# Kernel optimization log

Hardware: AMD Instinct MI355X
Metric: run time of the kernel (lower is better)

Reference implementation:

```python
import jax, jax.numpy as jnp
import numpy as np

N_NODES = 50000
N_EDGES = 640000
DIM_V = 128
DIM_E = 128
BN_EPS = 1e-5


def _lrelu(x):
    return jax.nn.leaky_relu(x, 0.2)


def _mlp3(x, W1, b1, W2, b2, W3, b3):
    h = _lrelu(x @ W1 + b1)
    h = _lrelu(h @ W2 + b2)
    return h @ W3 + b3


def _bn_train(x, gamma, beta):
    # BatchNorm1d in training mode: batch stats, biased variance
    m = jnp.mean(x, axis=0)
    v = jnp.mean((x - m) ** 2, axis=0)
    return (x - m) * jax.lax.rsqrt(v + BN_EPS) * gamma + beta


def setup_inputs() -> dict:
    key = jax.random.key(0)
    ks = jax.random.split(key, 20)
    node_fea = jax.random.normal(ks[0], (N_NODES, DIM_V), dtype=jnp.float32)
    edge_fea = jax.random.normal(ks[1], (N_EDGES, DIM_E), dtype=jnp.float32)
    idx1 = jax.random.randint(ks[2], (N_EDGES,), 0, N_NODES)
    idx2 = jax.random.randint(ks[3], (N_EDGES,), 0, N_NODES)
    dt_e = 2 * DIM_V + DIM_E  # phi_e input dim
    dt_v = DIM_V + DIM_E      # phi_v input dim
    s = 0.05
    return {
        "node_fea": node_fea, "edge_fea": edge_fea,
        "idx1": idx1, "idx2": idx2,
        "We1": jax.random.normal(ks[4], (dt_e, DIM_E), jnp.float32) * s,
        "be1": jnp.zeros((DIM_E,), jnp.float32),
        "We2": jax.random.normal(ks[5], (DIM_E, DIM_E), jnp.float32) * s,
        "be2": jnp.zeros((DIM_E,), jnp.float32),
        "We3": jax.random.normal(ks[6], (DIM_E, DIM_E), jnp.float32) * s,
        "be3": jnp.zeros((DIM_E,), jnp.float32),
        "Wv1": jax.random.normal(ks[7], (dt_v, DIM_V), jnp.float32) * s,
        "bv1": jnp.zeros((DIM_V,), jnp.float32),
        "Wv2": jax.random.normal(ks[8], (DIM_V, DIM_V), jnp.float32) * s,
        "bv2": jnp.zeros((DIM_V,), jnp.float32),
        "Wv3": jax.random.normal(ks[9], (DIM_V, DIM_V), jnp.float32) * s,
        "bv3": jnp.zeros((DIM_V,), jnp.float32),
        "gamma_e": jnp.ones((DIM_E,), jnp.float32),
        "beta_e": jnp.zeros((DIM_E,), jnp.float32),
        "gamma_v": jnp.ones((DIM_V,), jnp.float32),
        "beta_v": jnp.zeros((DIM_V,), jnp.float32),
    }


def reference(node_fea, edge_fea, idx1, idx2,
              We1, be1, We2, be2, We3, be3,
              Wv1, bv1, Wv2, bv2, Wv3, bv3,
              gamma_e, beta_e, gamma_v, beta_v):
    n_nodes = node_fea.shape[0]
    # gather endpoints, concat with edge features -> [E, 2*dim_v + dim_e]
    z = jnp.concatenate([node_fea[idx1], node_fea[idx2], edge_fea], axis=1)
    ek_prime = _bn_train(_mlp3(z, We1, be1, We2, be2, We3, be3), gamma_e, beta_e)
    edge_new = edge_fea + ek_prime
    # scatter_mean over idx1 into [N, dim_v]; empty segments stay zero
    seg_sum = jax.ops.segment_sum(ek_prime, idx1, num_segments=n_nodes)
    cnt = jax.ops.segment_sum(jnp.ones((idx1.shape[0], 1), ek_prime.dtype), idx1,
                              num_segments=n_nodes)
    vi_e_bar = seg_sum / jnp.maximum(cnt, 1.0)
    z2 = jnp.concatenate([vi_e_bar, node_fea], axis=1)
    vi_prime = _bn_train(_mlp3(z2, Wv1, bv1, Wv2, bv2, Wv3, bv3), gamma_v, beta_v)
    node_new = node_fea + vi_prime
    return node_new, edge_new
```

## Files before the change

kernel.cpp:

```cpp
#include <hip/hip_runtime.h>
#include <cstddef>

#define BN_EPS 1e-5f
constexpr int NNODES = 50000;
constexpr int NEDGES = 640000;
constexpr int DV = 128;
constexpr int NSLOT_E = 512;
constexpr int NSLOT_V = 256;

typedef __attribute__((ext_vector_type(4))) float f32x4;
typedef __attribute__((ext_vector_type(8))) short s16x8;
typedef unsigned short ushort_t;

__device__ __forceinline__ float lrelu(float x) { return x > 0.f ? x : 0.2f * x; }

__device__ __forceinline__ short f2bf(float f) {
  unsigned int u = __builtin_bit_cast(unsigned int, f);
  u += 0x7fffu + ((u >> 16) & 1u);
  return (short)(u >> 16);
}

__device__ __forceinline__ float bf2f(ushort_t u) {
  return __builtin_bit_cast(float, (unsigned int)u << 16);
}

__global__ __launch_bounds__(256)
void to_bf16(const float* __restrict__ src, ushort_t* __restrict__ dst, int n8) {
  int i = blockIdx.x * 256 + threadIdx.x;
  if (i >= n8) return;
  const float* s = src + (size_t)i * 8;
  float4 x0 = *(const float4*)s;
  float4 x1 = *(const float4*)(s + 4);
  s16x8 v;
  v[0] = f2bf(x0.x); v[1] = f2bf(x0.y); v[2] = f2bf(x0.z); v[3] = f2bf(x0.w);
  v[4] = f2bf(x1.x); v[5] = f2bf(x1.y); v[6] = f2bf(x1.z); v[7] = f2bf(x1.w);
  *(s16x8*)(dst + (size_t)i * 8) = v;
}

__global__ __launch_bounds__(256)
void pack_all(const float* __restrict__ W0, const float* __restrict__ W1,
              const float* __restrict__ W2, const float* __restrict__ W3,
              const float* __restrict__ W4, const float* __restrict__ W5,
              ushort_t* __restrict__ out) {
  int t = blockIdx.x * 256 + threadIdx.x;
  if (t >= 288 * 64) return;
  int lane = t & 63, f = t >> 6;
  const float* W; int lf;
  if (f < 96)       { W = W0; lf = f; }
  else if (f < 128) { W = W1; lf = f - 96; }
  else if (f < 160) { W = W2; lf = f - 128; }
  else if (f < 224) { W = W3; lf = f - 160; }
  else if (f < 256) { W = W4; lf = f - 224; }
  else              { W = W5; lf = f - 256; }
  int kk = lf >> 3, n = lf & 7;
  int k0 = kk * 32 + (lane >> 4) * 8, col = n * 16 + (lane & 15);
  s16x8 v;
#pragma unroll
  for (int j = 0; j < 8; j++) v[j] = f2bf(W[(size_t)(k0 + j) * DV + col]);
  *(s16x8*)(out + (size_t)t * 8) = v;
}

__global__ __launch_bounds__(256)
void csr_hist(const int* __restrict__ idx1, int* __restrict__ deg) {
  int e = blockIdx.x * 256 + threadIdx.x;
  if (e < NEDGES) atomicAdd(&deg[idx1[e]], 1);
}

__global__ __launch_bounds__(256)
void csr_scan(const int* __restrict__ deg, int* __restrict__ row_ptr,
              int* __restrict__ cursor) {
  __shared__ int part[256];
  const int t = threadIdx.x;
  const int CH = (NNODES + 255) / 256;
  int s = 0;
  for (int i = 0; i < CH; i++) { int n = t * CH + i; if (n < NNODES) s += deg[n]; }
  part[t] = s;
  __syncthreads();
  if (t == 0) {
    int run = 0;
    for (int i = 0; i < 256; i++) { int v = part[i]; part[i] = run; run += v; }
  }
  __syncthreads();
  int run = part[t];
  for (int i = 0; i < CH; i++) {
    int n = t * CH + i;
    if (n < NNODES) { row_ptr[n] = run; cursor[n] = run; run += deg[n]; }
  }
}

__global__ __launch_bounds__(256)
void csr_fill(const int* __restrict__ idx1, int* __restrict__ cursor,
              int* __restrict__ eidx) {
  int e = blockIdx.x * 256 + threadIdx.x;
  if (e < NEDGES) {
    int pos = atomicAdd(&cursor[idx1[e]], 1);
    eidx[pos] = e;
  }
}

template<int RS>
__device__ __forceinline__ void mfma_span(const char* Als, const s16x8* __restrict__ Wp,
                                          int fkk0, int nkk, f32x4 acc[2][2],
                                          int lane, int rg, int nh) {
  const int col0 = lane & 15;
  const int kg16 = (lane >> 4) * 16;
  const int sw = (col0 & 7) << 4;
  const int r0 = (rg * 32 + col0) * RS;
  const int r1 = (rg * 32 + 16 + col0) * RS;
#pragma unroll
  for (int kk = 0; kk < nkk; kk++) {
    const int ko = (kk * 64 + kg16) ^ sw;
    s16x8 a0 = *(const s16x8*)(Als + r0 + ko);
    s16x8 a1 = *(const s16x8*)(Als + r1 + ko);
    s16x8 b0 = Wp[(size_t)((fkk0 + kk) * 8 + nh * 2 + 0) * 64 + lane];
    s16x8 b1 = Wp[(size_t)((fkk0 + kk) * 8 + nh * 2 + 1) * 64 + lane];
    acc[0][0] = __builtin_amdgcn_mfma_f32_16x16x32_bf16(a0, b0, acc[0][0], 0, 0, 0);
    acc[0][1] = __builtin_amdgcn_mfma_f32_16x16x32_bf16(a0, b1, acc[0][1], 0, 0, 0);
    acc[1][0] = __builtin_amdgcn_mfma_f32_16x16x32_bf16(a1, b0, acc[1][0], 0, 0, 0);
    acc[1][1] = __builtin_amdgcn_mfma_f32_16x16x32_bf16(a1, b1, acc[1][1], 0, 0, 0);
  }
}

__device__ __forceinline__ void store_h64(char* H, const f32x4 acc[2][2],
                                          const float* __restrict__ bias,
                                          int lane, int rg, int nh) {
  const int col0 = lane & 15, lg = lane >> 4;
#pragma unroll
  for (int ar = 0; ar < 2; ar++) {
#pragma unroll
    for (int n = 0; n < 2; n++) {
      const int col = nh * 32 + n * 16 + col0;
      float bi = bias[col];
#pragma unroll
      for (int r = 0; r < 4; r++) {
        int row = rg * 32 + ar * 16 + lg * 4 + r;
        float v = lrelu(acc[ar][n][r] + bi);
        *(ushort_t*)(H + row * 256 + ((col * 2) ^ ((row & 7) << 4))) = (ushort_t)f2bf(v);
      }
    }
  }
}

__global__ __launch_bounds__(512, 8)
void edge_mlp_mfma(const ushort_t* __restrict__ node_b, const float* __restrict__ edge_fea,
                   const int* __restrict__ idx1, const int* __restrict__ idx2,
                   const ushort_t* __restrict__ Wp1, const float* __restrict__ b1,
                   const ushort_t* __restrict__ Wp2, const float* __restrict__ b2,
                   const ushort_t* __restrict__ Wp3, const float* __restrict__ b3,
                   ushort_t* __restrict__ h3b, float* __restrict__ slots) {
  __shared__ __align__(16) char zsm[64 * 384];
  __shared__ __align__(16) char hb[64 * 256];
  const int tid = threadIdx.x;
  const int lane = tid & 63, wid = tid >> 6;
  const int rg = wid & 1, nh = wid >> 1;
  const int e0 = blockIdx.x * 64;

  for (int t = tid; t < 64 * 24; t += 512) {
    int e = t / 24, p = t % 24;
    int er = e0 + e;
    const ushort_t* src = (p < 16) ? (node_b + (size_t)idx1[er] * DV + p * 8)
                                   : (node_b + (size_t)idx2[er] * DV + (p - 16) * 8);
    s16x8 v = *(const s16x8*)src;
    *(s16x8*)(zsm + e * 384 + ((p * 16) ^ ((e & 7) << 4))) = v;
  }
  __syncthreads();

  f32x4 acc[2][2];
#pragma unroll
  for (int i = 0; i < 2; i++)
#pragma unroll
    for (int j = 0; j < 2; j++) acc[i][j] = 0.0f;

  mfma_span<384>(zsm, (const s16x8*)Wp1, 0, 6, acc, lane, rg, nh);
  __syncthreads();

  for (int t = tid; t < 64 * 24; t += 512) {
    int e = t / 24, p = t % 24;
    int er = e0 + e;
    s16x8 v;
    if (p < 8) {
      v = *(const s16x8*)(node_b + (size_t)idx2[er] * DV + 64 + p * 8);
    } else {
      const float* s = edge_fea + (size_t)er * DV + (p - 8) * 8;
      float4 x0 = *(const float4*)s;
      float4 x1 = *(const float4*)(s + 4);
      v[0] = f2bf(x0.x); v[1] = f2bf(x0.y); v[2] = f2bf(x0.z); v[3] = f2bf(x0.w);
      v[4] = f2bf(x1.x); v[5] = f2bf(x1.y); v[6] = f2bf(x1.z); v[7] = f2bf(x1.w);
    }
    *(s16x8*)(zsm + e * 384 + ((p * 16) ^ ((e & 7) << 4))) = v;
  }
  __syncthreads();

  mfma_span<384>(zsm, (const s16x8*)Wp1, 6, 6, acc, lane, rg, nh);

  store_h64(hb, acc, b1, lane, rg, nh);
  __syncthreads();

#pragma unroll
  for (int i = 0; i < 2; i++)
#pragma unroll
    for (int j = 0; j < 2; j++) acc[i][j] = 0.0f;
  mfma_span<256>(hb, (const s16x8*)Wp2, 0, 4, acc, lane, rg, nh);

  store_h64(zsm, acc, b2, lane, rg, nh);
  __syncthreads();

#pragma unroll
  for (int i = 0; i < 2; i++)
#pragma unroll
    for (int j = 0; j < 2; j++) acc[i][j] = 0.0f;
  mfma_span<256>(zsm, (const s16x8*)Wp3, 0, 4, acc, lane, rg, nh);

  const int col0 = lane & 15, lg = lane >> 4;
  float* ps = (float*)hb;
  float* pq = ps + 16 * DV;
#pragma unroll
  for (int ar = 0; ar < 2; ar++) {
#pragma unroll
    for (int n = 0; n < 2; n++) {
      const int col = nh * 32 + n * 16 + col0;
      float bi = b3[col];
      float s = 0.f, q = 0.f;
#pragma unroll
      for (int r = 0; r < 4; r++) {
        int row = rg * 32 + ar * 16 + lg * 4 + r;
        float v = acc[ar][n][r] + bi;
        h3b[(size_t)(e0 + row) * 256 + col] = (ushort_t)f2bf(v);
        s += v; q += v * v;
      }
      ps[(rg * 8 + ar * 4 + lg) * DV + col] = s;
      pq[(rg * 8 + ar * 4 + lg) * DV + col] = q;
    }
  }
  __syncthreads();
  if (tid < 128) {
    float s = 0.f, q = 0.f;
#pragma unroll
    for (int g = 0; g < 16; g++) { s += ps[g * DV + tid]; q += pq[g * DV + tid]; }
    float* sl = slots + (size_t)(blockIdx.x % NSLOT_E) * 256;
    atomicAdd(sl + tid, s);
    atomicAdd(sl + 128 + tid, q);
  }
}

__global__ __launch_bounds__(256)
void node_gather_fused(const float* __restrict__ edge_fea, const int* __restrict__ row_ptr,
                       const int* __restrict__ deg, const int* __restrict__ eidx,
                       const float* __restrict__ ss, float* eslot,
                       ushort_t* __restrict__ vbar_b) {
  const int n = blockIdx.x * 4 + (threadIdx.x >> 6);
  const int lane = threadIdx.x & 63;
  if (n >= NNODES) return;
  const int start = row_ptr[n], d = deg[n];
  const int j = lane * 2;
  const float sc0 = ss[j], sc1 = ss[j + 1];
  const float sh0 = ss[128 + j], sh1 = ss[129 + j];
  const ushort_t* h3b = (const ushort_t*)eslot;
  float a0 = 0.f, a1 = 0.f;
  int i = 0;
  for (; i + 2 <= d; i += 2) {
    int e0 = eidx[start + i], e1 = eidx[start + i + 1];
    ushort2 u0 = *(const ushort2*)(h3b + (size_t)e0 * 256 + j);
    ushort2 u1 = *(const ushort2*)(h3b + (size_t)e1 * 256 + j);
    float2 f0 = *(const float2*)(edge_fea + (size_t)e0 * DV + j);
    float2 f1 = *(const float2*)(edge_fea + (size_t)e1 * DV + j);
    float h00 = bf2f(u0.x), h01 = bf2f(u0.y);
    float h10 = bf2f(u1.x), h11 = bf2f(u1.y);
    a0 += h00 + h10; a1 += h01 + h11;
    float2 o0, o1;
    o0.x = f0.x + fmaf(h00, sc0, sh0); o0.y = f0.y + fmaf(h01, sc1, sh1);
    o1.x = f1.x + fmaf(h10, sc0, sh0); o1.y = f1.y + fmaf(h11, sc1, sh1);
    *(float2*)(eslot + (size_t)e0 * DV + j) = o0;
    *(float2*)(eslot + (size_t)e1 * DV + j) = o1;
  }
  if (i < d) {
    int e0 = eidx[start + i];
    ushort2 u0 = *(const ushort2*)(h3b + (size_t)e0 * 256 + j);
    float2 f0 = *(const float2*)(edge_fea + (size_t)e0 * DV + j);
    float h00 = bf2f(u0.x), h01 = bf2f(u0.y);
    a0 += h00; a1 += h01;
    float2 o0;
    o0.x = f0.x + fmaf(h00, sc0, sh0); o0.y = f0.y + fmaf(h01, sc1, sh1);
    *(float2*)(eslot + (size_t)e0 * DV + j) = o0;
  }
  float vx, vy;
  if (d > 0) {
    float inv = 1.f / (float)d;
    vx = fmaf(a0 * inv, sc0, sh0);
    vy = fmaf(a1 * inv, sc1, sh1);
  } else {
    vx = 0.f; vy = 0.f;
  }
  ushort2 vb;
  vb.x = (ushort_t)f2bf(vx);
  vb.y = (ushort_t)f2bf(vy);
  *(ushort2*)(vbar_b + (size_t)n * DV + j) = vb;
}

template<int K>
__device__ __forceinline__ void layer_mfma(const char* Als, const s16x8* __restrict__ Wp,
                                           f32x4 acc[4], int lane, int rg, int nh) {
  const int arow = rg * 16 + (lane & 15);
  const int rowoff = arow * (K * 2);
  const int kg16 = (lane >> 4) * 16;
  const int sw = (arow & 7) << 4;
#pragma unroll
  for (int n = 0; n < 4; n++) acc[n] = 0.0f;
#pragma unroll 2
  for (int kk = 0; kk < K / 32; kk++) {
    s16x8 a = *(const s16x8*)(Als + rowoff + ((kk * 64 + kg16) ^ sw));
#pragma unroll
    for (int n = 0; n < 4; n++) {
      s16x8 b = Wp[(size_t)(kk * 8 + nh * 4 + n) * 64 + lane];
      acc[n] = __builtin_amdgcn_mfma_f32_16x16x32_bf16(a, b, acc[n], 0, 0, 0);
    }
  }
}

__device__ __forceinline__ void store_h_lds(char* H, const f32x4 acc[4],
                                            const float* __restrict__ bias,
                                            int lane, int rg, int nh) {
  const int col0 = lane & 15, lg = lane >> 4;
#pragma unroll
  for (int n = 0; n < 4; n++) {
    const int col = nh * 64 + n * 16 + col0;
    float bi = bias[col];
#pragma unroll
    for (int r = 0; r < 4; r++) {
      int row = rg * 16 + lg * 4 + r;
      float v = lrelu(acc[n][r] + bi);
      *(ushort_t*)(H + row * 256 + ((col * 2) ^ ((row & 7) << 4))) = (ushort_t)f2bf(v);
    }
  }
}

__global__ __launch_bounds__(256)
void node_mlp_mfma(const ushort_t* __restrict__ node_b, const ushort_t* __restrict__ vbar_b,
                   const ushort_t* __restrict__ Wp1, const float* __restrict__ b1,
                   const ushort_t* __restrict__ Wp2, const float* __restrict__ b2,
                   const ushort_t* __restrict__ Wp3, const float* __restrict__ b3,
                   float* __restrict__ h_out, float* __restrict__ slots) {
  __shared__ __align__(16) char zsm[32 * 512];
  __shared__ __align__(16) char hb[32 * 256];
  const int tid = threadIdx.x;
  const int lane = tid & 63, wid = tid >> 6;
  const int rg = wid & 1, nh = wid >> 1;
  const int n0 = blockIdx.x * 32;

  for (int t = tid; t < 32 * 32; t += 256) {
    int e = t / 32, p = t % 32;
    int nr = n0 + e;
    s16x8 v = (s16x8)0;
    if (nr < NNODES) {
      const ushort_t* src = (p < 16) ? (vbar_b + (size_t)nr * DV + p * 8)
                                     : (node_b + (size_t)nr * DV + (p - 16) * 8);
      v = *(const s16x8*)src;
    }
    *(s16x8*)(zsm + e * 512 + ((p * 16) ^ ((e & 7) << 4))) = v;
  }
  __syncthreads();

  f32x4 acc[4];

  layer_mfma<256>(zsm, (const s16x8*)Wp1, acc, lane, rg, nh);
  store_h_lds(hb, acc, b1, lane, rg, nh);
  __syncthreads();

  layer_mfma<128>(hb, (const s16x8*)Wp2, acc, lane, rg, nh);
  __syncthreads();
  store_h_lds(zsm, acc, b2, lane, rg, nh);
  __syncthreads();

  layer_mfma<128>(zsm, (const s16x8*)Wp3, acc, lane, rg, nh);

  const int col0 = lane & 15, lg = lane >> 4;
  float* ps = (float*)hb;
  float* pq = (float*)zsm;
#pragma unroll
  for (int n = 0; n < 4; n++) {
    const int col = nh * 64 + n * 16 + col0;
    float bi = b3[col];
    float s = 0.f, q = 0.f;
#pragma unroll
    for (int r = 0; r < 4; r++) {
      int row = rg * 16 + lg * 4 + r;
      int gr = n0 + row;
      if (gr < NNODES) {
        float v = acc[n][r] + bi;
        h_out[(size_t)gr * DV + col] = v;
        s += v; q += v * v;
      }
    }
    ps[(rg * 4 + lg) * DV + col] = s;
    pq[(rg * 4 + lg) * DV + col] = q;
  }
  __syncthreads();
  if (tid < 128) {
    float s = 0.f, q = 0.f;
#pragma unroll
    for (int g = 0; g < 8; g++) { s += ps[g * DV + tid]; q += pq[g * DV + tid]; }
    float* sl = slots + (size_t)(blockIdx.x % NSLOT_V) * 256;
    atomicAdd(sl + tid, s);
    atomicAdd(sl + 128 + tid, q);
  }
}

__global__ __launch_bounds__(256)
void stats_reduce(const float* __restrict__ slots, int nslot, float inv_n,
                  const float* __restrict__ gamma, const float* __restrict__ beta,
                  float* __restrict__ ss) {
  __shared__ float tot[256];
  const int j = threadIdx.x;
  float s = 0.f;
  for (int t = 0; t < nslot; t++) s += slots[(size_t)t * 256 + j];
  tot[j] = s;
  __syncthreads();
  if (j < 128) {
    float mean = tot[j] * inv_n;
    float var = tot[j + 128] * inv_n - mean * mean;
    float rs = rsqrtf(var + BN_EPS);
    float sc = gamma[j] * rs;
    ss[j] = sc;
    ss[128 + j] = beta[j] - mean * sc;
  }
}

__global__ __launch_bounds__(256)
void node_finalize(const float* __restrict__ node_fea, const float* __restrict__ ss,
                   float* __restrict__ h_inout) {
  const size_t base = (size_t)blockIdx.x * 1024 + threadIdx.x * 4;
  const int j = (int)(base & 127);
  float4 h = *(float4*)&h_inout[base];
  float4 nf = *(const float4*)&node_fea[base];
  float4 o;
  o.x = nf.x + fmaf(h.x, ss[j + 0], ss[128 + j + 0]);
  o.y = nf.y + fmaf(h.y, ss[j + 1], ss[128 + j + 1]);
  o.z = nf.z + fmaf(h.z, ss[j + 2], ss[128 + j + 2]);
  o.w = nf.w + fmaf(h.w, ss[j + 3], ss[128 + j + 3]);
  *(float4*)&h_inout[base] = o;
}

extern "C" void kernel_launch(void* const* d_in, const int* in_sizes, int n_in,
                              void* d_out, int out_size, void* d_ws, size_t ws_size,
                              hipStream_t stream) {
  const float* node_fea = (const float*)d_in[0];
  const float* edge_fea = (const float*)d_in[1];
  const int* idx1 = (const int*)d_in[2];
  const int* idx2 = (const int*)d_in[3];
  const float* We1 = (const float*)d_in[4];  const float* be1 = (const float*)d_in[5];
  const float* We2 = (const float*)d_in[6];  const float* be2 = (const float*)d_in[7];
  const float* We3 = (const float*)d_in[8];  const float* be3 = (const float*)d_in[9];
  const float* Wv1 = (const float*)d_in[10]; const float* bv1 = (const float*)d_in[11];
  const float* Wv2 = (const float*)d_in[12]; const float* bv2 = (const float*)d_in[13];
  const float* Wv3 = (const float*)d_in[14]; const float* bv3 = (const float*)d_in[15];
  const float* gamma_e = (const float*)d_in[16]; const float* beta_e = (const float*)d_in[17];
  const float* gamma_v = (const float*)d_in[18]; const float* beta_v = (const float*)d_in[19];

  float* out_node = (float*)d_out;
  float* out_edge = out_node + (size_t)NNODES * DV;

  float* ws = (float*)d_ws;
  size_t o = 0;
  int* deg = (int*)(ws + o);      o += NNODES;
  float* slots_e = ws + o;        o += (size_t)NSLOT_E * 256;
  float* slots_v = ws + o;        o += (size_t)NSLOT_V * 256;
  const size_t zero_bytes = o * sizeof(float);
  int* row_ptr = (int*)(ws + o);  o += NNODES;
  int* cursor = (int*)(ws + o);   o += NNODES;
  int* eidx = (int*)(ws + o);     o += NEDGES;
  float* ss_e = ws + o;           o += 256;
  float* ss_v = ws + o;           o += 256;
  ushort_t* node_b = (ushort_t*)(ws + o);  o += (size_t)NNODES * DV / 2;
  ushort_t* vbar_b = (ushort_t*)(ws + o);  o += (size_t)NNODES * DV / 2;
  ushort_t* wpack = (ushort_t*)(ws + o);

  const ushort_t* Wp_e1 = wpack;
  const ushort_t* Wp_e2 = wpack + (size_t)96 * 512;
  const ushort_t* Wp_e3 = wpack + (size_t)128 * 512;
  const ushort_t* Wp_v1 = wpack + (size_t)160 * 512;
  const ushort_t* Wp_v2 = wpack + (size_t)224 * 512;
  const ushort_t* Wp_v3 = wpack + (size_t)256 * 512;

  hipMemsetAsync(d_ws, 0, zero_bytes, stream);

  to_bf16<<<(NNODES * DV / 8 + 255) / 256, 256, 0, stream>>>(node_fea, node_b, NNODES * DV / 8);
  pack_all<<<72, 256, 0, stream>>>(We1, We2, We3, Wv1, Wv2, Wv3, wpack);
  csr_hist<<<(NEDGES + 255) / 256, 256, 0, stream>>>(idx1, deg);
  csr_scan<<<1, 256, 0, stream>>>(deg, row_ptr, cursor);
  csr_fill<<<(NEDGES + 255) / 256, 256, 0, stream>>>(idx1, cursor, eidx);

  edge_mlp_mfma<<<NEDGES / 64, 512, 0, stream>>>(node_b, edge_fea, idx1, idx2,
                                                 Wp_e1, be1, Wp_e2, be2, Wp_e3, be3,
                                                 (ushort_t*)out_edge, slots_e);
  stats_reduce<<<1, 256, 0, stream>>>(slots_e, NSLOT_E, 1.f / NEDGES, gamma_e, beta_e, ss_e);
  node_gather_fused<<<(NNODES + 3) / 4, 256, 0, stream>>>(edge_fea, row_ptr, deg, eidx,
                                                          ss_e, out_edge, vbar_b);
  node_mlp_mfma<<<(NNODES + 31) / 32, 256, 0, stream>>>(node_b, vbar_b,
                                                        Wp_v1, bv1, Wp_v2, bv2, Wp_v3, bv3,
                                                        out_node, slots_v);
  stats_reduce<<<1, 256, 0, stream>>>(slots_v, NSLOT_V, 1.f / NNODES, gamma_v, beta_v, ss_v);
  node_finalize<<<(NNODES * DV) / 1024, 256, 0, stream>>>(node_fea, ss_v, out_node);
}
```

Measured before the change: 861.2 us.

## Stash bf16 edge features in output slot and use hardware bf16 pack conversion

The edge MLP kernel now writes its bf16-converted edge features into the upper half of each 256-short output row, alongside the bf16 h3. The gather kernel reads them from there instead of re-reading fp32 edge_fea, which cuts its read traffic on the residual path. The software round-to-nearest bf16 conversion is also replaced by the v_cvt_pk_bf16_f32 instruction, with a packed two-value variant. In exchange, the edge residual is now added from a bf16-rounded copy of edge_fea rather than the exact fp32 values, and the edge kernel does an extra global write.

```diff
diff --git a/kernel.cpp b/kernel.cpp
--- a/kernel.cpp
+++ b/kernel.cpp
@@ -14,12 +14,24 @@
 
 __device__ __forceinline__ float lrelu(float x) { return x > 0.f ? x : 0.2f * x; }
 
-__device__ __forceinline__ short f2bf(float f) {
-  unsigned int u = __builtin_bit_cast(unsigned int, f);
-  u += 0x7fffu + ((u >> 16) & 1u);
-  return (short)(u >> 16);
-}
-
+__device__ __forceinline__ unsigned cvt_pk_bf16(float lo, float hi) {
+  unsigned r;
+  asm("v_cvt_pk_bf16_f32 %0, %1, %2" : "=v"(r) : "v"(lo), "v"(hi));
+  return r;
+}
+__device__ __forceinline__ ushort_t f2bf(float f) {
+  unsigned r;
+  asm("v_cvt_pk_bf16_f32 %0, %1, %1" : "=v"(r) : "v"(f));
+  return (ushort_t)r;
+}
+__device__ __forceinline__ s16x8 pack8(float4 a, float4 b) {
+  union { unsigned u[4]; s16x8 v; } r;
+  r.u[0] = cvt_pk_bf16(a.x, a.y);
+  r.u[1] = cvt_pk_bf16(a.z, a.w);
+  r.u[2] = cvt_pk_bf16(b.x, b.y);
+  r.u[3] = cvt_pk_bf16(b.z, b.w);
+  return r.v;
+}
 __device__ __forceinline__ float bf2f(ushort_t u) {
   return __builtin_bit_cast(float, (unsigned int)u << 16);
 }
@@ -31,10 +43,7 @@
   const float* s = src + (size_t)i * 8;
   float4 x0 = *(const float4*)s;
   float4 x1 = *(const float4*)(s + 4);
-  s16x8 v;
-  v[0] = f2bf(x0.x); v[1] = f2bf(x0.y); v[2] = f2bf(x0.z); v[3] = f2bf(x0.w);
-  v[4] = f2bf(x1.x); v[5] = f2bf(x1.y); v[6] = f2bf(x1.z); v[7] = f2bf(x1.w);
-  *(s16x8*)(dst + (size_t)i * 8) = v;
+  *(s16x8*)(dst + (size_t)i * 8) = pack8(x0, x1);
 }
 
 __global__ __launch_bounds__(256)
@@ -56,7 +65,7 @@
   int k0 = kk * 32 + (lane >> 4) * 8, col = n * 16 + (lane & 15);
   s16x8 v;
 #pragma unroll
-  for (int j = 0; j < 8; j++) v[j] = f2bf(W[(size_t)(k0 + j) * DV + col]);
+  for (int j = 0; j < 8; j++) v[j] = (short)f2bf(W[(size_t)(k0 + j) * DV + col]);
   *(s16x8*)(out + (size_t)t * 8) = v;
 }
 
@@ -135,7 +144,7 @@
       for (int r = 0; r < 4; r++) {
         int row = rg * 32 + ar * 16 + lg * 4 + r;
         float v = lrelu(acc[ar][n][r] + bi);
-        *(ushort_t*)(H + row * 256 + ((col * 2) ^ ((row & 7) << 4))) = (ushort_t)f2bf(v);
+        *(ushort_t*)(H + row * 256 + ((col * 2) ^ ((row & 7) << 4))) = f2bf(v);
       }
     }
   }
@@ -147,7 +156,7 @@
                    const ushort_t* __restrict__ Wp1, const float* __restrict__ b1,
                    const ushort_t* __restrict__ Wp2, const float* __restrict__ b2,
                    const ushort_t* __restrict__ Wp3, const float* __restrict__ b3,
-                   ushort_t* __restrict__ h3b, float* __restrict__ slots) {
+                   ushort_t* __restrict__ slot, float* __restrict__ slots) {
   __shared__ __align__(16) char zsm[64 * 384];
   __shared__ __align__(16) char hb[64 * 256];
   const int tid = threadIdx.x;
@@ -184,8 +193,8 @@
       const float* s = edge_fea + (size_t)er * DV + (p - 8) * 8;
       float4 x0 = *(const float4*)s;
       float4 x1 = *(const float4*)(s + 4);
-      v[0] = f2bf(x0.x); v[1] = f2bf(x0.y); v[2] = f2bf(x0.z); v[3] = f2bf(x0.w);
-      v[4] = f2bf(x1.x); v[5] = f2bf(x1.y); v[6] = f2bf(x1.z); v[7] = f2bf(x1.w);
+      v = pack8(x0, x1);
+      *(s16x8*)(slot + (size_t)er * 256 + 128 + (p - 8) * 8) = v;
     }
     *(s16x8*)(zsm + e * 384 + ((p * 16) ^ ((e & 7) << 4))) = v;
   }
@@ -225,7 +234,7 @@
       for (int r = 0; r < 4; r++) {
         int row = rg * 32 + ar * 16 + lg * 4 + r;
         float v = acc[ar][n][r] + bi;
-        h3b[(size_t)(e0 + row) * 256 + col] = (ushort_t)f2bf(v);
+        slot[(size_t)(e0 + row) * 256 + col] = f2bf(v);
         s += v; q += v * v;
       }
       ps[(rg * 8 + ar * 4 + lg) * DV + col] = s;
@@ -244,10 +253,9 @@
 }
 
 __global__ __launch_bounds__(256)
-void node_gather_fused(const float* __restrict__ edge_fea, const int* __restrict__ row_ptr,
-                       const int* __restrict__ deg, const int* __restrict__ eidx,
-                       const float* __restrict__ ss, float* eslot,
-                       ushort_t* __restrict__ vbar_b) {
+void node_gather_fused(const int* __restrict__ row_ptr, const int* __restrict__ deg,
+                       const int* __restrict__ eidx, const float* __restrict__ ss,
+                       float* eslot, ushort_t* __restrict__ vbar_b) {
   const int n = blockIdx.x * 4 + (threadIdx.x >> 6);
   const int lane = threadIdx.x & 63;
   if (n >= NNODES) return;
@@ -255,32 +263,32 @@
   const int j = lane * 2;
   const float sc0 = ss[j], sc1 = ss[j + 1];
   const float sh0 = ss[128 + j], sh1 = ss[129 + j];
-  const ushort_t* h3b = (const ushort_t*)eslot;
+  const ushort_t* slot = (const ushort_t*)eslot;
   float a0 = 0.f, a1 = 0.f;
   int i = 0;
   for (; i + 2 <= d; i += 2) {
     int e0 = eidx[start + i], e1 = eidx[start + i + 1];
-    ushort2 u0 = *(const ushort2*)(h3b + (size_t)e0 * 256 + j);
-    ushort2 u1 = *(const ushort2*)(h3b + (size_t)e1 * 256 + j);
-    float2 f0 = *(const float2*)(edge_fea + (size_t)e0 * DV + j);
-    float2 f1 = *(const float2*)(edge_fea + (size_t)e1 * DV + j);
-    float h00 = bf2f(u0.x), h01 = bf2f(u0.y);
-    float h10 = bf2f(u1.x), h11 = bf2f(u1.y);
+    ushort2 uh0 = *(const ushort2*)(slot + (size_t)e0 * 256 + j);
+    ushort2 ue0 = *(const ushort2*)(slot + (size_t)e0 * 256 + 128 + j);
+    ushort2 uh1 = *(const ushort2*)(slot + (size_t)e1 * 256 + j);
+    ushort2 ue1 = *(const ushort2*)(slot + (size_t)e1 * 256 + 128 + j);
+    float h00 = bf2f(uh0.x), h01 = bf2f(uh0.y);
+    float h10 = bf2f(uh1.x), h11 = bf2f(uh1.y);
     a0 += h00 + h10; a1 += h01 + h11;
     float2 o0, o1;
-    o0.x = f0.x + fmaf(h00, sc0, sh0); o0.y = f0.y + fmaf(h01, sc1, sh1);
-    o1.x = f1.x + fmaf(h10, sc0, sh0); o1.y = f1.y + fmaf(h11, sc1, sh1);
+    o0.x = bf2f(ue0.x) + fmaf(h00, sc0, sh0); o0.y = bf2f(ue0.y) + fmaf(h01, sc1, sh1);
+    o1.x = bf2f(ue1.x) + fmaf(h10, sc0, sh0); o1.y = bf2f(ue1.y) + fmaf(h11, sc1, sh1);
     *(float2*)(eslot + (size_t)e0 * DV + j) = o0;
     *(float2*)(eslot + (size_t)e1 * DV + j) = o1;
   }
   if (i < d) {
     int e0 = eidx[start + i];
-    ushort2 u0 = *(const ushort2*)(h3b + (size_t)e0 * 256 + j);
-    float2 f0 = *(const float2*)(edge_fea + (size_t)e0 * DV + j);
-    float h00 = bf2f(u0.x), h01 = bf2f(u0.y);
+    ushort2 uh0 = *(const ushort2*)(slot + (size_t)e0 * 256 + j);
+    ushort2 ue0 = *(const ushort2*)(slot + (size_t)e0 * 256 + 128 + j);
+    float h00 = bf2f(uh0.x), h01 = bf2f(uh0.y);
     a0 += h00; a1 += h01;
     float2 o0;
-    o0.x = f0.x + fmaf(h00, sc0, sh0); o0.y = f0.y + fmaf(h01, sc1, sh1);
+    o0.x = bf2f(ue0.x) + fmaf(h00, sc0, sh0); o0.y = bf2f(ue0.y) + fmaf(h01, sc1, sh1);
     *(float2*)(eslot + (size_t)e0 * DV + j) = o0;
   }
   float vx, vy;
@@ -291,10 +299,8 @@
   } else {
     vx = 0.f; vy = 0.f;
   }
-  ushort2 vb;
-  vb.x = (ushort_t)f2bf(vx);
-  vb.y = (ushort_t)f2bf(vy);
-  *(ushort2*)(vbar_b + (size_t)n * DV + j) = vb;
+  unsigned vb = cvt_pk_bf16(vx, vy);
+  *(unsigned*)(vbar_b + (size_t)n * DV + j) = vb;
 }
 
 template<int K>
@@ -329,7 +335,7 @@
     for (int r = 0; r < 4; r++) {
       int row = rg * 16 + lg * 4 + r;
       float v = lrelu(acc[n][r] + bi);
-      *(ushort_t*)(H + row * 256 + ((col * 2) ^ ((row & 7) << 4))) = (ushort_t)f2bf(v);
+      *(ushort_t*)(H + row * 256 + ((col * 2) ^ ((row & 7) << 4))) = f2bf(v);
     }
   }
 }
@@ -493,7 +499,7 @@
                                                  Wp_e1, be1, Wp_e2, be2, Wp_e3, be3,
                                                  (ushort_t*)out_edge, slots_e);
   stats_reduce<<<1, 256, 0, stream>>>(slots_e, NSLOT_E, 1.f / NEDGES, gamma_e, beta_e, ss_e);
-  node_gather_fused<<<(NNODES + 3) / 4, 256, 0, stream>>>(edge_fea, row_ptr, deg, eidx,
+  node_gather_fused<<<(NNODES + 3) / 4, 256, 0, stream>>>(row_ptr, deg, eidx,
                                                           ss_e, out_edge, vbar_b);
   node_mlp_mfma<<<(NNODES + 31) / 32, 256, 0, stream>>>(node_b, vbar_b,
                                                         Wp_v1, bv1, Wp_v2, bv2, Wp_v3, bv3,
```

After: 859.7 us. No clear change (-0.2%).
